# Performance work log

Hardware: AMD Instinct MI355X
Metric: run time of the kernel (lower is better)

## Reference

```python
import jax, jax.numpy as jnp
import numpy as np
import math

B, S, D, K = 8, 2048, 1024, 64
EPS = 1e-5

def _ln(x):
    m = jnp.mean(x, axis=-1, keepdims=True)
    v = jnp.mean((x - m) ** 2, axis=-1, keepdims=True)
    return (x - m) * jax.lax.rsqrt(v + EPS)

def setup_inputs() -> dict:
    key = jax.random.key(0)
    ks = jax.random.split(key, 14)
    s = 0.02
    return {
        "x":  jax.random.normal(ks[0], (B, S, D), dtype=jnp.float32),
        "Wk": jax.random.normal(ks[1], (D, K), dtype=jnp.float32) * s,
        "bk": jnp.zeros((K,), dtype=jnp.float32),
        "Wq": jax.random.normal(ks[2], (D, K), dtype=jnp.float32) * s,
        "bq": jnp.zeros((K,), dtype=jnp.float32),
        "Wv": jax.random.normal(ks[3], (D, D), dtype=jnp.float32) * s,
        "bv": jnp.zeros((D,), dtype=jnp.float32),
        "Wb": jax.random.normal(ks[4], (D, 1), dtype=jnp.float32) * s,
        "bb": jnp.zeros((1,), dtype=jnp.float32),
        "W1": jax.random.normal(ks[5], (D, D), dtype=jnp.float32) * s,
        "b1": jnp.zeros((D,), dtype=jnp.float32),
        "g1": jnp.ones((D,), dtype=jnp.float32),
        "be1": jnp.zeros((D,), dtype=jnp.float32),
    }

def reference(x, Wk, bk, Wq, bq, Wv, bv, Wb, bb, W1, b1, g1, be1):
    scale = 1.0 / math.sqrt(K)
    keys    = (jnp.einsum('bsd,dk->bsk', x, Wk) + bk) * scale   # [B,S,K]
    queries = jnp.einsum('bsd,dk->bsk', x, Wq) + bq             # [B,S,K]
    values  = jnp.einsum('bsd,de->bse', x, Wv) + bv             # [B,S,D]
    biases  = jnp.einsum('bsd,do->bso', x, Wb) + bb             # [B,S,1]
    # scores[b,i,j] = keys[b,i] . queries[b,j] + biases[b,i]
    scores = jax.nn.sigmoid(jnp.einsum('bik,bjk->bij', keys, queries) + biases)
    attention = jnp.einsum('bij,bjd->bid', scores, values)      # [B,S,D]
    res = _ln(x + attention) * g1 + be1
    feedforward = jax.nn.relu(jnp.einsum('bsd,de->bse', res, W1) + b1)
    return _ln(res + feedforward)
```

## Files before the change

kernel.cpp:

```cpp
#include <hip/hip_runtime.h>
#include <math.h>


typedef __bf16 bf16_t;
typedef __bf16 bf16x2_t __attribute__((ext_vector_type(2)));
typedef __bf16 bf16x4_t __attribute__((ext_vector_type(4)));
typedef __bf16 bf16x8_t __attribute__((ext_vector_type(8)));
typedef float  f32x4    __attribute__((ext_vector_type(4)));

#define DEV static __device__ __forceinline__

DEV void gll16(const void* g, void* l) {
  __builtin_amdgcn_global_load_lds(
      (const __attribute__((address_space(1))) void*)g,
      (__attribute__((address_space(3))) void*)l, 16, 0, 0);
}

template <int MODE, int MFAST>
__global__ __launch_bounds__(512, 2) void gemm256(
    const bf16_t* __restrict__ A, const bf16_t* __restrict__ B,
    bf16_t* __restrict__ C, int K, int lda, int ldb, int ldc,
    long sAb, long sBb, long sCb, const float* __restrict__ aux0) {
  const int gx = gridDim.x, gy = gridDim.y;
  const int gxy = gx * gy;
  const int nwg = gxy * (int)gridDim.z;
  const int orig = blockIdx.x + gx * blockIdx.y + gxy * blockIdx.z;
  const int lid = (orig & 7) * (nwg >> 3) + (orig >> 3);
  const int bz = lid / gxy;
  const int rem = lid - bz * gxy;
  const int bx = MFAST ? (rem / gy) : (rem % gx);
  const int by = MFAST ? (rem % gy) : (rem / gx);

  A += (long)bz * sAb;
  B += (long)bz * sBb;
  const int m0 = by * 256, n0 = bx * 256;

  __shared__ bf16_t As[2][2][256 * 32];
  __shared__ bf16_t Bs[2][2][256 * 32];

  const int tid = threadIdx.x;
  const int wid = tid >> 6, l = tid & 63;
  const int wr = wid >> 2, wc = wid & 3;
  const int lr = l & 15, lh = l >> 4;

  const int sRow = tid >> 2;
  const int sSl = (tid & 3) ^ ((tid >> 3) & 3);
  const bf16_t* Asrc = A + (long)(m0 + sRow) * lda + sSl * 8;
  const bf16_t* Bsrc = B + (long)(n0 + sRow) * ldb + sSl * 8;
  const long aStep = (long)128 * lda, bStep = (long)128 * ldb;

#define STAGE_A(b, h, kt) do { \
    const bf16_t* s_ = Asrc + (kt) * 64 + (h) * 32; \
    gll16(s_,         &As[b][h][tid * 8]); \
    gll16(s_ + aStep, &As[b][h][4096 + tid * 8]); } while (0)
#define STAGE_B(b, h, kt) do { \
    const bf16_t* s_ = Bsrc + (kt) * 64 + (h) * 32; \
    gll16(s_,         &Bs[b][h][tid * 8]); \
    gll16(s_ + bStep, &Bs[b][h][4096 + tid * 8]); } while (0)

  const int sw = (lh ^ ((lr >> 1) & 3)) * 8;
  const int aOff = (wr * 128 + lr) * 32 + sw;
  const int bOff = (wc * 64 + lr) * 32 + sw;

  f32x4 acc[8][4] = {};
  const int NT = K >> 6;

  STAGE_A(0, 0, 0); STAGE_B(0, 0, 0); STAGE_A(0, 1, 0); STAGE_B(0, 1, 0);
  asm volatile("s_waitcnt vmcnt(4)" ::: "memory");
  __builtin_amdgcn_s_barrier();

  for (int t = 0; t < NT; ++t) {
    const int p = t & 1, q = p ^ 1;
    const bool pf = (t + 1 < NT);

    bf16x8_t bF[4], aF[4];
#pragma unroll
    for (int n = 0; n < 4; ++n) bF[n] = *(const bf16x8_t*)&Bs[p][0][bOff + n * 512];
#pragma unroll
    for (int m = 0; m < 4; ++m) aF[m] = *(const bf16x8_t*)&As[p][0][aOff + m * 512];
    if (pf) STAGE_A(q, 0, t + 1);
    __builtin_amdgcn_s_barrier();
    asm volatile("s_waitcnt lgkmcnt(0)" ::: "memory");
    __builtin_amdgcn_sched_barrier(0);
    __builtin_amdgcn_s_setprio(1);
#pragma unroll
    for (int m = 0; m < 4; ++m)
#pragma unroll
      for (int n = 0; n < 4; ++n)
        acc[m][n] = __builtin_amdgcn_mfma_f32_16x16x32_bf16(aF[m], bF[n], acc[m][n], 0, 0, 0);
    __builtin_amdgcn_s_setprio(0);
    __builtin_amdgcn_s_barrier();

    bf16x8_t aG[4];
#pragma unroll
    for (int m = 0; m < 4; ++m) aG[m] = *(const bf16x8_t*)&As[p][0][aOff + (m + 4) * 512];
    if (pf) {
      STAGE_B(q, 0, t + 1);
      asm volatile("s_waitcnt vmcnt(4)" ::: "memory");
    } else {
      asm volatile("s_waitcnt vmcnt(0)" ::: "memory");
    }
    __builtin_amdgcn_s_barrier();
    asm volatile("s_waitcnt lgkmcnt(0)" ::: "memory");
    __builtin_amdgcn_sched_barrier(0);
    __builtin_amdgcn_s_setprio(1);
#pragma unroll
    for (int m = 0; m < 4; ++m)
#pragma unroll
      for (int n = 0; n < 4; ++n)
        acc[m + 4][n] = __builtin_amdgcn_mfma_f32_16x16x32_bf16(aG[m], bF[n], acc[m + 4][n], 0, 0, 0);
    __builtin_amdgcn_s_setprio(0);
    __builtin_amdgcn_s_barrier();

#pragma unroll
    for (int n = 0; n < 4; ++n) bF[n] = *(const bf16x8_t*)&Bs[p][1][bOff + n * 512];
#pragma unroll
    for (int m = 0; m < 4; ++m) aF[m] = *(const bf16x8_t*)&As[p][1][aOff + m * 512];
    if (pf) STAGE_A(q, 1, t + 1);
    __builtin_amdgcn_s_barrier();
    asm volatile("s_waitcnt lgkmcnt(0)" ::: "memory");
    __builtin_amdgcn_sched_barrier(0);
    __builtin_amdgcn_s_setprio(1);
#pragma unroll
    for (int m = 0; m < 4; ++m)
#pragma unroll
      for (int n = 0; n < 4; ++n)
        acc[m][n] = __builtin_amdgcn_mfma_f32_16x16x32_bf16(aF[m], bF[n], acc[m][n], 0, 0, 0);
    __builtin_amdgcn_s_setprio(0);
    __builtin_amdgcn_s_barrier();

#pragma unroll
    for (int m = 0; m < 4; ++m) aG[m] = *(const bf16x8_t*)&As[p][1][aOff + (m + 4) * 512];
    if (pf) STAGE_B(q, 1, t + 1);
    asm volatile("s_waitcnt vmcnt(4)" ::: "memory");
    __builtin_amdgcn_s_barrier();
    asm volatile("s_waitcnt lgkmcnt(0)" ::: "memory");
    __builtin_amdgcn_sched_barrier(0);
    __builtin_amdgcn_s_setprio(1);
#pragma unroll
    for (int m = 0; m < 4; ++m)
#pragma unroll
      for (int n = 0; n < 4; ++n)
        acc[m + 4][n] = __builtin_amdgcn_mfma_f32_16x16x32_bf16(aG[m], bF[n], acc[m + 4][n], 0, 0, 0);
    __builtin_amdgcn_s_setprio(0);
    __builtin_amdgcn_s_barrier();
  }
#undef STAGE_A
#undef STAGE_B

  bf16_t* Cb = C + (long)bz * sCb;
  const int rowb = m0 + wr * 128 + lh * 4;
  const int colb = n0 + wc * 64 + lr;
#pragma unroll
  for (int m = 0; m < 8; ++m)
#pragma unroll
    for (int n = 0; n < 4; ++n) {
      const f32x4 v = acc[m][n];
      const int cc = colb + n * 16;
#pragma unroll
      for (int r = 0; r < 4; ++r) {
        const int rr = rowb + m * 16 + r;
        const float val = v[r];
        if constexpr (MODE == 1) {
          Cb[(long)rr * ldc + cc] = (bf16_t)(val + aux0[rr]);
        } else if constexpr (MODE == 3) {
          Cb[(long)rr * ldc + cc] = (bf16_t)val;
        } else {
          Cb[(long)rr * ldc + cc] = (bf16_t)fmaxf(val + aux0[cc], 0.0f);
        }
      }
    }
}

template <int MODE, int MFAST>
__global__ __launch_bounds__(256) void gemm_bt(
    const bf16_t* __restrict__ A, const bf16_t* __restrict__ B,
    void* __restrict__ Cv, int M, int N, int K, int lda, int ldb, int ldc,
    long sAb, long sBb, long sCb,
    const float* __restrict__ aux0, const float* __restrict__ aux1, long sAux) {
  const int gx = gridDim.x, gy = gridDim.y;
  const int gxy = gx * gy;
  const int nwg = gxy * (int)gridDim.z;
  const int orig = blockIdx.x + gx * blockIdx.y + gxy * blockIdx.z;
  const int q = nwg >> 3, r8 = nwg & 7;
  const int xcd = orig & 7, seq = orig >> 3;
  const int lid = (xcd < r8 ? xcd * (q + 1) : r8 * (q + 1) + (xcd - r8) * q) + seq;
  const int bz = lid / gxy;
  const int rem = lid - bz * gxy;
  const int bx = MFAST ? (rem / gy) : (rem % gx);
  const int by = MFAST ? (rem % gy) : (rem / gx);

  A += (long)bz * sAb;
  B += (long)bz * sBb;
  const float* a0 = (MODE == 2) ? (aux0 + (long)bz * sAux) : aux0;

  const int m0 = by * 128;
  const int n0 = bx * 128;

  __shared__ bf16_t As[2][128 * 32];
  __shared__ bf16_t Bs[2][128 * 32];

  const int tid = threadIdx.x;
  const int w = tid >> 6, l = tid & 63;
  const int wr = w >> 1, wc = w & 1;
  const int lr = l & 15, lh = l >> 4;

  const int srow = l >> 2;
  const int scol = (((l & 3) ^ (srow & 3)) << 3);

  f32x4 acc[4][4] = {};

  auto stage = [&](int buf, int k0) {
#pragma unroll
    for (int half = 0; half < 2; ++half) {
      const int i = 2 * w + half;
      const int row = (i << 4) + srow;
      gll16(A + (long)(m0 + row) * lda + k0 + scol, &As[buf][i << 9]);
      gll16(B + (long)(n0 + row) * ldb + k0 + scol, &Bs[buf][i << 9]);
    }
  };

  stage(0, 0);
  __syncthreads();
  int cur = 0;
  const int sw = ((lh ^ (lr & 3)) << 3);

  for (int k0 = 0; k0 < K; k0 += 32) {
    if (k0 + 32 < K) stage(cur ^ 1, k0 + 32);

    bf16x8_t af[4], bfm[4];
#pragma unroll
    for (int m = 0; m < 4; ++m)
      af[m] = *(const bf16x8_t*)(&As[cur][(((wr << 6) + (m << 4) + lr) << 5) + sw]);
#pragma unroll
    for (int n = 0; n < 4; ++n)
      bfm[n] = *(const bf16x8_t*)(&Bs[cur][(((wc << 6) + (n << 4) + lr) << 5) + sw]);
#pragma unroll
    for (int m = 0; m < 4; ++m)
#pragma unroll
      for (int n = 0; n < 4; ++n)
        acc[m][n] = __builtin_amdgcn_mfma_f32_16x16x32_bf16(af[m], bfm[n], acc[m][n], 0, 0, 0);

    __syncthreads();
    cur ^= 1;
  }

  const int rowbase = m0 + (wr << 6) + (lh << 2);
  const int colbase = n0 + (wc << 6) + lr;
#pragma unroll
  for (int m = 0; m < 4; ++m) {
#pragma unroll
    for (int n = 0; n < 4; ++n) {
      const f32x4 v = acc[m][n];
      const int cc = colbase + (n << 4);
#pragma unroll
      for (int r = 0; r < 4; ++r) {
        const int rr = rowbase + (m << 4) + r;
        const float val = v[r];
        if constexpr (MODE == 0) {
          const float b = (cc < 64) ? aux0[cc] : aux1[cc - 64];
          const float s = (cc < 64) ? 0.125f : 1.0f;
          ((bf16_t*)Cv)[(long)rr * ldc + cc] = (bf16_t)((val + b) * s);
        } else {
          const float zz = val + a0[rr];
          const float e = __expf(-zz);
          const float sg = __builtin_amdgcn_rcpf(1.0f + e);
          ((bf16_t*)Cv)[(long)bz * sCb + (long)rr * ldc + cc] = (bf16_t)sg;
        }
      }
    }
  }
}

__global__ __launch_bounds__(256) void cast_bf16_kernel(
    const float* __restrict__ in, bf16_t* __restrict__ out, long n) {
  long i = ((long)blockIdx.x * 256 + threadIdx.x) * 4;
  const long step = (long)gridDim.x * 1024;
  for (; i < n; i += step) {
    const float4 v = *(const float4*)(in + i);
    bf16x4_t o;
    o[0] = (bf16_t)v.x; o[1] = (bf16_t)v.y; o[2] = (bf16_t)v.z; o[3] = (bf16_t)v.w;
    *(bf16x4_t*)(out + i) = o;
  }
}

__global__ __launch_bounds__(256) void transpose_cast_kernel(
    const float* __restrict__ in, bf16_t* __restrict__ out, int R, int C) {
  __shared__ float t[32][33];
  const int c0 = blockIdx.x * 32, r0 = blockIdx.y * 32;
  const int tx = threadIdx.x & 31, ty = threadIdx.x >> 5;
#pragma unroll
  for (int i = 0; i < 4; ++i) {
    const int rl = ty * 4 + i;
    t[rl][tx] = in[(long)(r0 + rl) * C + c0 + tx];
  }
  __syncthreads();
#pragma unroll
  for (int i = 0; i < 4; ++i) {
    const int rl = ty * 4 + i;
    out[(long)(c0 + rl) * R + r0 + tx] = (bf16_t)t[tx][rl];
  }
}

__global__ __launch_bounds__(256) void bias_kernel(
    const bf16_t* __restrict__ x, const float* __restrict__ Wb,
    const float* __restrict__ bb, float* __restrict__ biases) {
  const int r = blockIdx.x * 4 + (threadIdx.x >> 6);
  const int l = threadIdx.x & 63;
  const bf16_t* xr = x + (long)r * 1024;
  float s = 0.f;
#pragma unroll
  for (int i = 0; i < 8; ++i) {
    const bf16x2_t v = *(const bf16x2_t*)(xr + (l << 1) + (i << 7));
    const float2 wv = *(const float2*)(Wb + (l << 1) + (i << 7));
    s += (float)v[0] * wv.x + (float)v[1] * wv.y;
  }
#pragma unroll
  for (int off = 1; off < 64; off <<= 1) s += __shfl_xor(s, off);
  if (l == 0) biases[r] = s + bb[0];
}

DEV float2 block_sum2(float s, float ss) {
#pragma unroll
  for (int off = 1; off < 64; off <<= 1) {
    s += __shfl_xor(s, off);
    ss += __shfl_xor(ss, off);
  }
  __shared__ float bs[4], bss[4];
  const int w = threadIdx.x >> 6, l = threadIdx.x & 63;
  if (l == 0) { bs[w] = s; bss[w] = ss; }
  __syncthreads();
  s = bs[0] + bs[1] + bs[2] + bs[3];
  ss = bss[0] + bss[1] + bss[2] + bss[3];
  return make_float2(s, ss);
}

__global__ __launch_bounds__(256) void ln1_kernel(
    const bf16_t* __restrict__ x, const bf16_t* __restrict__ attn,
    const float* __restrict__ g, const float* __restrict__ be,
    bf16_t* __restrict__ res) {
  const long r = blockIdx.x;
  const int t = threadIdx.x;
  const bf16x4_t xv = *(const bf16x4_t*)(x + r * 1024 + t * 4);
  const bf16x4_t av = *(const bf16x4_t*)(attn + r * 1024 + t * 4);
  const float y0 = (float)xv[0] + (float)av[0], y1 = (float)xv[1] + (float)av[1];
  const float y2 = (float)xv[2] + (float)av[2], y3 = (float)xv[3] + (float)av[3];
  const float2 s2 = block_sum2(y0 + y1 + y2 + y3, y0 * y0 + y1 * y1 + y2 * y2 + y3 * y3);
  const float mean = s2.x * (1.0f / 1024.0f);
  const float var = s2.y * (1.0f / 1024.0f) - mean * mean;
  const float rs = rsqrtf(var + 1e-5f);
  const int c = t * 4;
  bf16x4_t o;
  o[0] = (bf16_t)((y0 - mean) * rs * g[c + 0] + be[c + 0]);
  o[1] = (bf16_t)((y1 - mean) * rs * g[c + 1] + be[c + 1]);
  o[2] = (bf16_t)((y2 - mean) * rs * g[c + 2] + be[c + 2]);
  o[3] = (bf16_t)((y3 - mean) * rs * g[c + 3] + be[c + 3]);
  *(bf16x4_t*)(res + r * 1024 + c) = o;
}

__global__ __launch_bounds__(256) void ln2_kernel(
    const bf16_t* __restrict__ res, const bf16_t* __restrict__ h,
    float* __restrict__ out) {
  const long r = blockIdx.x;
  const int t = threadIdx.x;
  const bf16x4_t rv = *(const bf16x4_t*)(res + r * 1024 + t * 4);
  const bf16x4_t hv = *(const bf16x4_t*)(h + r * 1024 + t * 4);
  const float y0 = (float)rv[0] + (float)hv[0], y1 = (float)rv[1] + (float)hv[1];
  const float y2 = (float)rv[2] + (float)hv[2], y3 = (float)rv[3] + (float)hv[3];
  const float2 s2 = block_sum2(y0 + y1 + y2 + y3, y0 * y0 + y1 * y1 + y2 * y2 + y3 * y3);
  const float mean = s2.x * (1.0f / 1024.0f);
  const float var = s2.y * (1.0f / 1024.0f) - mean * mean;
  const float rs = rsqrtf(var + 1e-5f);
  float4 o;
  o.x = (y0 - mean) * rs; o.y = (y1 - mean) * rs;
  o.z = (y2 - mean) * rs; o.w = (y3 - mean) * rs;
  ((float4*)(out + r * 1024))[t] = o;
}

extern "C" void kernel_launch(void* const* d_in, const int* in_sizes, int n_in,
                              void* d_out, int out_size, void* d_ws, size_t ws_size,
                              hipStream_t stream) {
  const float* x   = (const float*)d_in[0];
  const float* Wk  = (const float*)d_in[1];
  const float* bk  = (const float*)d_in[2];
  const float* Wq  = (const float*)d_in[3];
  const float* bq  = (const float*)d_in[4];
  const float* Wv  = (const float*)d_in[5];
  const float* bv  = (const float*)d_in[6];
  const float* Wb  = (const float*)d_in[7];
  const float* bb  = (const float*)d_in[8];
  const float* W1  = (const float*)d_in[9];
  const float* b1  = (const float*)d_in[10];
  const float* g1  = (const float*)d_in[11];
  const float* be1 = (const float*)d_in[12];
  float* out = (float*)d_out;

  char* ws = (char*)d_ws;
  bf16_t* x_bf    = (bf16_t*)(ws + 0);
  bf16_t* vt_bf   = (bf16_t*)(ws + 33554432);
  bf16_t* kq_bf   = (bf16_t*)(ws + 67108864);
  bf16_t* Wkqt    = (bf16_t*)(ws + 71303168);
  bf16_t* Wvt     = (bf16_t*)(ws + 71565312);
  bf16_t* W1t     = (bf16_t*)(ws + 73662464);
  float*  biases  = (float*) (ws + 75759616);
  bf16_t* scores  = (bf16_t*)(ws + 75825152);
  bf16_t* attn_bf = (bf16_t*)(ws + 142934016);
  bf16_t* res_bf  = (bf16_t*)(ws + 176488448);
  bf16_t* h_bf    = attn_bf;

  const long BS = 16384;

  cast_bf16_kernel<<<8192, 256, 0, stream>>>(x, x_bf, BS * 1024);
  transpose_cast_kernel<<<dim3(2, 32), 256, 0, stream>>>(Wk, Wkqt, 1024, 64);
  transpose_cast_kernel<<<dim3(2, 32), 256, 0, stream>>>(Wq, Wkqt + 64 * 1024, 1024, 64);
  transpose_cast_kernel<<<dim3(32, 32), 256, 0, stream>>>(Wv, Wvt, 1024, 1024);
  transpose_cast_kernel<<<dim3(32, 32), 256, 0, stream>>>(W1, W1t, 1024, 1024);
  bias_kernel<<<4096, 256, 0, stream>>>(x_bf, Wb, bb, biases);

  gemm_bt<0, 0><<<dim3(1, 128, 1), 256, 0, stream>>>(
      x_bf, Wkqt, kq_bf, 16384, 128, 1024, 1024, 1024, 128, 0, 0, 0, bk, bq, 0);

  gemm256<1, 1><<<dim3(64, 4, 1), 512, 0, stream>>>(
      Wvt, x_bf, vt_bf, 1024, 1024, 1024, 16384, 0, 0, 0, bv);

  gemm_bt<2, 0><<<dim3(16, 16, 8), 256, 0, stream>>>(
      kq_bf, kq_bf + 64, scores, 2048, 2048, 64, 128, 128, 2048,
      2048L * 128, 2048L * 128, 2048L * 2048, biases, nullptr, 2048);

  gemm256<3, 0><<<dim3(4, 8, 8), 512, 0, stream>>>(
      scores, vt_bf, attn_bf, 2048, 2048, 16384, 1024,
      2048L * 2048, 2048, 2048L * 1024, nullptr);

  ln1_kernel<<<16384, 256, 0, stream>>>(x_bf, attn_bf, g1, be1, res_bf);

  gemm256<4, 0><<<dim3(4, 64, 1), 512, 0, stream>>>(
      res_bf, W1t, h_bf, 1024, 1024, 1024, 1024, 0, 0, 0, b1);

  ln2_kernel<<<16384, 256, 0, stream>>>(res_bf, h_bf, out);
}
```

Before: 263.1 us.

## Cut barriers in GEMM main loop and overlap LDS fragment loads with MFMA

Restructures the bf16 GEMM main loop so each K-tile half uses one barrier at its start instead of four. The second A fragment set (aG) is now read from LDS before the first MFMA block, gated by a partial lgkmcnt wait, so the second block's LDS reads overlap the first block's MFMAs. The B prefetch is moved to sit between the two MFMA blocks. The aim is to remove synchronisation stalls and expose more load/compute overlap. The cost is more live fragment registers and a looser wait/barrier scheme that depends on exact vmcnt accounting for correctness.

```diff
diff --git a/kernel.cpp b/kernel.cpp
--- a/kernel.cpp
+++ b/kernel.cpp
@@ -66,87 +66,67 @@
   const int NT = K >> 6;
 
   STAGE_A(0, 0, 0); STAGE_B(0, 0, 0); STAGE_A(0, 1, 0); STAGE_B(0, 1, 0);
-  asm volatile("s_waitcnt vmcnt(4)" ::: "memory");
-  __builtin_amdgcn_s_barrier();
+
+#define MFMA_LO() do { \
+    __builtin_amdgcn_s_setprio(1); \
+    _Pragma("unroll") for (int m = 0; m < 4; ++m) \
+    _Pragma("unroll") for (int n = 0; n < 4; ++n) \
+      acc[m][n] = __builtin_amdgcn_mfma_f32_16x16x32_bf16(aF[m], bF[n], acc[m][n], 0, 0, 0); \
+    __builtin_amdgcn_s_setprio(0); } while (0)
+#define MFMA_HI() do { \
+    __builtin_amdgcn_s_setprio(1); \
+    _Pragma("unroll") for (int m = 0; m < 4; ++m) \
+    _Pragma("unroll") for (int n = 0; n < 4; ++n) \
+      acc[m + 4][n] = __builtin_amdgcn_mfma_f32_16x16x32_bf16(aG[m], bF[n], acc[m + 4][n], 0, 0, 0); \
+    __builtin_amdgcn_s_setprio(0); } while (0)
 
   for (int t = 0; t < NT; ++t) {
     const int p = t & 1, q = p ^ 1;
     const bool pf = (t + 1 < NT);
-
-    bf16x8_t bF[4], aF[4];
+    bf16x8_t bF[4], aF[4], aG[4];
+
+    asm volatile("s_waitcnt vmcnt(4)" ::: "memory");
+    __builtin_amdgcn_s_barrier();
 #pragma unroll
     for (int n = 0; n < 4; ++n) bF[n] = *(const bf16x8_t*)&Bs[p][0][bOff + n * 512];
 #pragma unroll
     for (int m = 0; m < 4; ++m) aF[m] = *(const bf16x8_t*)&As[p][0][aOff + m * 512];
     if (pf) STAGE_A(q, 0, t + 1);
-    __builtin_amdgcn_s_barrier();
+#pragma unroll
+    for (int m = 0; m < 4; ++m) aG[m] = *(const bf16x8_t*)&As[p][0][aOff + (m + 4) * 512];
+    asm volatile("s_waitcnt lgkmcnt(4)" ::: "memory");
+    __builtin_amdgcn_sched_barrier(0);
+    MFMA_LO();
+    if (pf) STAGE_B(q, 0, t + 1);
     asm volatile("s_waitcnt lgkmcnt(0)" ::: "memory");
     __builtin_amdgcn_sched_barrier(0);
-    __builtin_amdgcn_s_setprio(1);
-#pragma unroll
-    for (int m = 0; m < 4; ++m)
-#pragma unroll
-      for (int n = 0; n < 4; ++n)
-        acc[m][n] = __builtin_amdgcn_mfma_f32_16x16x32_bf16(aF[m], bF[n], acc[m][n], 0, 0, 0);
-    __builtin_amdgcn_s_setprio(0);
-    __builtin_amdgcn_s_barrier();
-
-    bf16x8_t aG[4];
-#pragma unroll
-    for (int m = 0; m < 4; ++m) aG[m] = *(const bf16x8_t*)&As[p][0][aOff + (m + 4) * 512];
+    MFMA_HI();
+
     if (pf) {
-      STAGE_B(q, 0, t + 1);
       asm volatile("s_waitcnt vmcnt(4)" ::: "memory");
     } else {
       asm volatile("s_waitcnt vmcnt(0)" ::: "memory");
     }
     __builtin_amdgcn_s_barrier();
+#pragma unroll
+    for (int n = 0; n < 4; ++n) bF[n] = *(const bf16x8_t*)&Bs[p][1][bOff + n * 512];
+#pragma unroll
+    for (int m = 0; m < 4; ++m) aF[m] = *(const bf16x8_t*)&As[p][1][aOff + m * 512];
+    if (pf) STAGE_A(q, 1, t + 1);
+#pragma unroll
+    for (int m = 0; m < 4; ++m) aG[m] = *(const bf16x8_t*)&As[p][1][aOff + (m + 4) * 512];
+    asm volatile("s_waitcnt lgkmcnt(4)" ::: "memory");
+    __builtin_amdgcn_sched_barrier(0);
+    MFMA_LO();
+    if (pf) STAGE_B(q, 1, t + 1);
     asm volatile("s_waitcnt lgkmcnt(0)" ::: "memory");
     __builtin_amdgcn_sched_barrier(0);
-    __builtin_amdgcn_s_setprio(1);
-#pragma unroll
-    for (int m = 0; m < 4; ++m)
-#pragma unroll
-      for (int n = 0; n < 4; ++n)
-        acc[m + 4][n] = __builtin_amdgcn_mfma_f32_16x16x32_bf16(aG[m], bF[n], acc[m + 4][n], 0, 0, 0);
-    __builtin_amdgcn_s_setprio(0);
-    __builtin_amdgcn_s_barrier();
-
-#pragma unroll
-    for (int n = 0; n < 4; ++n) bF[n] = *(const bf16x8_t*)&Bs[p][1][bOff + n * 512];
-#pragma unroll
-    for (int m = 0; m < 4; ++m) aF[m] = *(const bf16x8_t*)&As[p][1][aOff + m * 512];
-    if (pf) STAGE_A(q, 1, t + 1);
-    __builtin_amdgcn_s_barrier();
-    asm volatile("s_waitcnt lgkmcnt(0)" ::: "memory");
-    __builtin_amdgcn_sched_barrier(0);
-    __builtin_amdgcn_s_setprio(1);
-#pragma unroll
-    for (int m = 0; m < 4; ++m)
-#pragma unroll
-      for (int n = 0; n < 4; ++n)
-        acc[m][n] = __builtin_amdgcn_mfma_f32_16x16x32_bf16(aF[m], bF[n], acc[m][n], 0, 0, 0);
-    __builtin_amdgcn_s_setprio(0);
-    __builtin_amdgcn_s_barrier();
-
-#pragma unroll
-    for (int m = 0; m < 4; ++m) aG[m] = *(const bf16x8_t*)&As[p][1][aOff + (m + 4) * 512];
-    if (pf) STAGE_B(q, 1, t + 1);
-    asm volatile("s_waitcnt vmcnt(4)" ::: "memory");
-    __builtin_amdgcn_s_barrier();
-    asm volatile("s_waitcnt lgkmcnt(0)" ::: "memory");
-    __builtin_amdgcn_sched_barrier(0);
-    __builtin_amdgcn_s_setprio(1);
-#pragma unroll
-    for (int m = 0; m < 4; ++m)
-#pragma unroll
-      for (int n = 0; n < 4; ++n)
-        acc[m + 4][n] = __builtin_amdgcn_mfma_f32_16x16x32_bf16(aG[m], bF[n], acc[m + 4][n], 0, 0, 0);
-    __builtin_amdgcn_s_setprio(0);
-    __builtin_amdgcn_s_barrier();
+    MFMA_HI();
   }
 #undef STAGE_A
 #undef STAGE_B
+#undef MFMA_LO
+#undef MFMA_HI
 
   bf16_t* Cb = C + (long)bz * sCb;
   const int rowb = m0 + wr * 128 + lh * 4;
```

Result: no change. 264.7 us (+0.6%).
